# Kernel tuning notes

Measured on AMD Instinct MI355X. Metric: run time of the kernel, lower is better.

The kernel has to match this reference:

```python
import jax, jax.numpy as jnp
import numpy as np

B, N_RX, IMG_H, IMG_W = 128, 34, 512, 512
N_CAT = 5  # num_rx_categories + 1


def setup_inputs() -> dict:
    key = jax.random.key(0)
    k_pow, k_xy, k_cat, k_dw, k_db, k_cw, k_cb = jax.random.split(key, 7)
    # x_vecs columns: [power, x_coord, y_coord, category]
    powers = jax.random.normal(k_pow, (B, N_RX, 1), dtype=jnp.float32)
    coords = jax.random.randint(k_xy, (B, N_RX, 2), 0, IMG_W).astype(jnp.float32)
    cats = jax.random.randint(k_cat, (B, N_RX, 1), 0, N_CAT).astype(jnp.float32)
    x_vecs = jnp.concatenate([powers, coords, cats], axis=-1)  # [B, N_RX, 4]
    # learned per-device and per-category affine parameters (init: ones/zeros,
    # perturbed slightly so the test is non-trivial)
    device_weights = 1.0 + 0.1 * jax.random.normal(k_dw, (N_RX,), dtype=jnp.float32)
    device_bias = 0.1 * jax.random.normal(k_db, (N_RX,), dtype=jnp.float32)
    category_weights = 1.0 + 0.1 * jax.random.normal(k_cw, (N_CAT,), dtype=jnp.float32)
    category_bias = 0.1 * jax.random.normal(k_cb, (N_CAT,), dtype=jnp.float32)
    return {
        "x_vecs": x_vecs,
        "device_weights": device_weights,
        "device_bias": device_bias,
        "category_weights": category_weights,
        "category_bias": category_bias,
    }


def reference(x_vecs, device_weights, device_bias, category_weights, category_bias):
    batch, n_rx = x_vecs.shape[0], x_vecs.shape[1]
    raw_powers = x_vecs[:, :, 0]                      # [B, N]
    power_mask = (raw_powers != 0).astype(x_vecs.dtype)
    # per-device affine (device_multiplication)
    p = raw_powers * device_weights + power_mask * device_bias
    # per-category affine (category_multiplication)
    cat = x_vecs[:, :, -1].astype(jnp.int32)          # [B, N]
    p = p * category_weights[cat] + power_mask * category_bias[cat]
    # coordinate-based scatter into image grid
    coords = jnp.round(x_vecs[:, :, 1:3]).astype(jnp.int32)  # [B, N, 2] (x, y)
    b_idx = jnp.repeat(jnp.arange(batch), n_rx)
    yy = coords[:, :, 1].ravel()
    xx = coords[:, :, 0].ravel()
    x_img = jnp.zeros((batch, 2, IMG_H, IMG_W), dtype=x_vecs.dtype)
    x_img = x_img.at[b_idx, 0, yy, xx].set(p.ravel())
    x_img = x_img.at[b_idx, 1, yy, xx].set(raw_powers.ravel())
    return x_img
```

## Files before the change

kernel.cpp:

```cpp
#include <hip/hip_runtime.h>

#define B_BATCH 128
#define N_RX 34
#define IMG 512
#define N_CAT 5

__global__ void Vec2Im_scatter_kernel(const float* __restrict__ x_vecs,
                                      const float* __restrict__ device_weights,
                                      const float* __restrict__ device_bias,
                                      const float* __restrict__ category_weights,
                                      const float* __restrict__ category_bias,
                                      float* __restrict__ out) {
    int b = blockIdx.x * blockDim.x + threadIdx.x;
    if (b >= B_BATCH) return;

    const float4* xv = reinterpret_cast<const float4*>(x_vecs) + (size_t)b * N_RX;
    float* plane0 = out + (size_t)b * 2 * IMG * IMG;
    float* plane1 = plane0 + (size_t)IMG * IMG;

    for (int r = 0; r < N_RX; ++r) {
        float4 v = xv[r];
        float raw = v.x;
        float mask = (raw != 0.0f) ? 1.0f : 0.0f;
        float p = raw * device_weights[r] + mask * device_bias[r];
        int cat = (int)v.w;
        p = p * category_weights[cat] + mask * category_bias[cat];
        int xx = (int)rintf(v.y);
        int yy = (int)rintf(v.z);
        int off = yy * IMG + xx;
        plane0[off] = p;
        plane1[off] = raw;
    }
}

extern "C" void kernel_launch(void* const* d_in, const int* in_sizes, int n_in,
                              void* d_out, int out_size, void* d_ws, size_t ws_size,
                              hipStream_t stream) {
    const float* x_vecs           = (const float*)d_in[0];
    const float* device_weights   = (const float*)d_in[1];
    const float* device_bias      = (const float*)d_in[2];
    const float* category_weights = (const float*)d_in[3];
    const float* category_bias    = (const float*)d_in[4];
    float* out = (float*)d_out;

    hipMemsetAsync(d_out, 0, (size_t)out_size * sizeof(float), stream);

    Vec2Im_scatter_kernel<<<1, 128, 0, stream>>>(
        x_vecs, device_weights, device_bias, category_weights, category_bias, out);
}
```

Measured before the change: 275.3 us.

## Fuse zero-fill and scatter into one chunked kernel per plane region

Replaces the separate device memset plus single-block serial scatter with one kernel where each block zeroes a 64-row chunk of one output plane using float4 stores, then scatters only receivers whose row falls inside that chunk. This removes the extra launch and the serialized scatter, and spreads the work over many blocks. Thread 0 rescans all receivers per block, which adds a little redundant work.

New measurement: 266.2 us. 3.3% less time.

```diff
diff --git a/kernel.cpp b/kernel.cpp
--- a/kernel.cpp
+++ b/kernel.cpp
@@ -5,31 +5,57 @@
 #define IMG 512
 #define N_CAT 5
 
-__global__ void Vec2Im_scatter_kernel(const float* __restrict__ x_vecs,
-                                      const float* __restrict__ device_weights,
-                                      const float* __restrict__ device_bias,
-                                      const float* __restrict__ category_weights,
-                                      const float* __restrict__ category_bias,
-                                      float* __restrict__ out) {
-    int b = blockIdx.x * blockDim.x + threadIdx.x;
-    if (b >= B_BATCH) return;
 
-    const float4* xv = reinterpret_cast<const float4*>(x_vecs) + (size_t)b * N_RX;
-    float* plane0 = out + (size_t)b * 2 * IMG * IMG;
-    float* plane1 = plane0 + (size_t)IMG * IMG;
+#define CHUNKS_PER_PLANE 8
+#define ROWS_PER_CHUNK (IMG / CHUNKS_PER_PLANE)
+#define FLOATS_PER_BLOCK (ROWS_PER_CHUNK * IMG)
+#define THREADS 256
+#define VEC4_PER_THREAD (FLOATS_PER_BLOCK / (THREADS * 4))
 
-    for (int r = 0; r < N_RX; ++r) {
-        float4 v = xv[r];
-        float raw = v.x;
-        float mask = (raw != 0.0f) ? 1.0f : 0.0f;
-        float p = raw * device_weights[r] + mask * device_bias[r];
-        int cat = (int)v.w;
-        p = p * category_weights[cat] + mask * category_bias[cat];
-        int xx = (int)rintf(v.y);
-        int yy = (int)rintf(v.z);
-        int off = yy * IMG + xx;
-        plane0[off] = p;
-        plane1[off] = raw;
+__global__ __launch_bounds__(THREADS)
+void Vec2Im_fused_kernel(const float* __restrict__ x_vecs,
+                         const float* __restrict__ device_weights,
+                         const float* __restrict__ device_bias,
+                         const float* __restrict__ category_weights,
+                         const float* __restrict__ category_bias,
+                         float* __restrict__ out) {
+    const int blk   = blockIdx.x;
+    const int chunk = blk & (CHUNKS_PER_PLANE - 1);
+    const int plane = (blk >> 3) & 1;
+    const int b     = blk >> 4;
+
+    const size_t plane_start = (size_t)(b * 2 + plane) * (IMG * IMG);
+    const size_t chunk_start = plane_start + (size_t)chunk * FLOATS_PER_BLOCK;
+
+    float4* out4 = reinterpret_cast<float4*>(out + chunk_start);
+    const float4 z = make_float4(0.f, 0.f, 0.f, 0.f);
+    const int tid = threadIdx.x;
+#pragma unroll
+    for (int i = 0; i < VEC4_PER_THREAD; ++i)
+        out4[i * THREADS + tid] = z;
+
+    __syncthreads();
+
+    if (tid == 0) {
+        const int row0 = chunk * ROWS_PER_CHUNK;
+        const float4* xv = reinterpret_cast<const float4*>(x_vecs) + (size_t)b * N_RX;
+        for (int r = 0; r < N_RX; ++r) {
+            float4 v = xv[r];
+            int yy = (int)rintf(v.z);
+            if (yy < row0 || yy >= row0 + ROWS_PER_CHUNK) continue;
+            int xx = (int)rintf(v.y);
+            float raw = v.x;
+            float val;
+            if (plane == 1) {
+                val = raw;
+            } else {
+                float mask = (raw != 0.0f) ? 1.0f : 0.0f;
+                float p = raw * device_weights[r] + mask * device_bias[r];
+                int cat = (int)v.w;
+                val = p * category_weights[cat] + mask * category_bias[cat];
+            }
+            out[plane_start + (size_t)(yy * IMG + xx)] = val;
+        }
     }
 }
 
@@ -43,8 +69,8 @@
     const float* category_bias    = (const float*)d_in[4];
     float* out = (float*)d_out;
 
-    hipMemsetAsync(d_out, 0, (size_t)out_size * sizeof(float), stream);
-
-    Vec2Im_scatter_kernel<<<1, 128, 0, stream>>>(
+    dim3 grid(B_BATCH * 2 * CHUNKS_PER_PLANE);
+    dim3 block(THREADS);
+    Vec2Im_fused_kernel<<<grid, block, 0, stream>>>(
         x_vecs, device_weights, device_bias, category_weights, category_bias, out);
 }
```
